# Performance work log

Measured on AMD Instinct MI355X. Metric: run time of the kernel, lower is better.

## Reference

```python
import jax, jax.numpy as jnp
import numpy as np

TEMP = 0.1
GAMMA = 0.75
CHUNK = 300      # hardcoded b=300 in the original forward
EPS = 1e-8
LOSS_WEIGHT = 0.1


def _l2norm(x, axis):
    return x / (jnp.linalg.norm(x, axis=axis, keepdims=True) + 1e-12)


def setup_inputs() -> dict:
    key = jax.random.key(0)
    k = jax.random.split(key, 6)
    B, D, C = 2, 128, 19
    H = W = 240          # full image -> n = 57600 negatives (192 chunks of 300)
    h = w = 60           # overlap crop size -> P = 3600 anchor pixels
    feats_view1 = _l2norm(jax.random.normal(k[0], (B, D, H, W), jnp.float32), axis=1)
    pos_feats1 = _l2norm(jax.random.normal(k[1], (B, D, h, w), jnp.float32), axis=1)
    pos_feats2 = _l2norm(jax.random.normal(k[2], (B, D, h, w), jnp.float32), axis=1)
    pseudo_logits1 = jax.random.uniform(k[3], (B, C, h, w), jnp.float32)
    pseudo_logits2 = jax.random.uniform(k[4], (B, C, h, w), jnp.float32)
    neg_pseudo_logits = jax.random.uniform(k[5], (B, C, H, W), jnp.float32)
    return {
        "feats_view1": feats_view1,
        "pos_feats1": pos_feats1,
        "pos_feats2": pos_feats2,
        "pseudo_logits1": pseudo_logits1,
        "pseudo_logits2": pseudo_logits2,
        "neg_pseudo_logits": neg_pseudo_logits,
    }


def _per_sample(f1, f2, nf, pl1, pl2, npl):
    # f1,f2: [D,h,w] cropped overlap feats; nf: [D,H,W] negatives; pl*: [C,h,w]; npl: [C,H,W]
    D = f1.shape[0]
    C = pl1.shape[0]
    feats1 = f1.reshape(D, -1)                               # [D, P]
    feats2 = jax.lax.stop_gradient(f2.reshape(D, -1))        # detach() in original
    P = feats1.shape[1]
    neg_feats = nf.reshape(D, -1)                            # [D, N]
    N = neg_feats.shape[1]
    labels1 = jnp.argmax(pl1.reshape(C, -1), axis=0)         # [P] anchor pseudo-labels
    neg_labels = jnp.argmax(npl.reshape(C, -1), axis=0)      # [N] negative pseudo-labels

    pos1 = (feats1 * feats2).sum(0) / TEMP                   # [P]

    nchunks = N // CHUNK                                     # N chosen divisible by CHUNK
    nf_c = neg_feats.reshape(D, nchunks, CHUNK).transpose(1, 0, 2)  # [K, D, b]
    nl_c = neg_labels.reshape(nchunks, CHUNK)                       # [K, b]

    def step(acc, xs):
        nfi, nli = xs
        scores = jnp.einsum('dp,db->pb', feats1, nfi) / TEMP        # [P, b]
        mask = (labels1[:, None] != nli[None, :]).astype(scores.dtype)
        return acc + (mask * jnp.exp(scores)).sum(-1), None

    neg_logits, _ = jax.lax.scan(step, jnp.zeros((P,), feats1.dtype), (nf_c, nl_c))

    pos_exp = jnp.exp(pos1)
    lossn = -jnp.log(pos_exp / (pos_exp + neg_logits + EPS) + EPS)  # [P]

    # mask1 = argmax over classes of (dir_mask * pos_mask), as in the original
    combo = ((pl1 < pl2) & (pl2 > GAMMA)).astype(lossn.dtype).reshape(C, -1)
    mask1 = jnp.argmax(combo, axis=0).astype(lossn.dtype)           # [P]
    return (mask1 * lossn).sum() / (mask1.sum() + EPS)


def reference(feats_view1, pos_feats1, pos_feats2, pseudo_logits1, pseudo_logits2, neg_pseudo_logits):
    losses = jax.vmap(_per_sample)(pos_feats1, pos_feats2, feats_view1,
                                   pseudo_logits1, pseudo_logits2, neg_pseudo_logits)
    return LOSS_WEIGHT * (losses[0] + losses[1])
```

## Files before the change

kernel.cpp:

```cpp
#include <hip/hip_runtime.h>
#include <string.h>

#define D_ 128
#define P_ 3600
#define N_ 57600
#define C_ 19
#define NB 2
#define NSPLIT 8
#define TOTCH 450
#define PT 29

typedef short bf16x8 __attribute__((ext_vector_type(8)));
typedef float f32x4 __attribute__((ext_vector_type(4)));

__device__ __forceinline__ ushort f2bf(float x) {
  unsigned u = __float_as_uint(x);
  u = (u + 0x7fffu + ((u >> 16) & 1u)) >> 16;
  return (ushort)u;
}

__device__ __forceinline__ void gload_lds16(const void* g, void* l) {
  __builtin_amdgcn_global_load_lds(
      (const __attribute__((address_space(1))) unsigned int*)g,
      (__attribute__((address_space(3))) unsigned int*)l, 16, 0, 0);
}

__global__ void prep_kernel(const float* __restrict__ XB, ushort* __restrict__ YB,
                            const float* __restrict__ XA, ushort* __restrict__ YA,
                            const float* __restrict__ npl, int* __restrict__ nlab,
                            const float* __restrict__ pl1, const float* __restrict__ pl2,
                            const float* __restrict__ f2,
                            int* __restrict__ lab1, float* __restrict__ mask1,
                            float* __restrict__ pos1, float* __restrict__ neg_logits) {
  __shared__ float T[64][129];
  const int b = blockIdx.y;
  const int tid = threadIdx.x;

  if (blockIdx.x >= N_ / 64 + 57) {
    int p = (blockIdx.x - (N_ / 64 + 57)) * 256 + tid;
    if (p >= P_) return;
    const float* a1 = pl1 + (size_t)b * C_ * P_ + p;
    const float* a2 = pl2 + (size_t)b * C_ * P_ + p;
    float best = a1[0]; int bi = 0;
    int mfirst = ((a1[0] < a2[0]) && (a2[0] > 0.75f)) ? 0 : -1;
#pragma unroll
    for (int c = 1; c < C_; ++c) {
      float v1 = a1[(size_t)c * P_], v2 = a2[(size_t)c * P_];
      if (v1 > best) { best = v1; bi = c; }
      if (mfirst < 0 && (v1 < v2) && (v2 > 0.75f)) mfirst = c;
    }
    lab1[b * P_ + p] = bi;
    mask1[b * P_ + p] = (mfirst < 0) ? 0.0f : (float)mfirst;
    neg_logits[b * P_ + p] = 0.0f;
    const float* g1 = XA + (size_t)b * D_ * P_ + p;
    const float* g2 = f2 + (size_t)b * D_ * P_ + p;
    float s = 0.f;
#pragma unroll 8
    for (int d = 0; d < D_; ++d) s += g1[(size_t)d * P_] * g2[(size_t)d * P_];
    pos1[b * P_ + p] = s * 10.0f;
    return;
  }

  const bool isB = blockIdx.x < (N_ / 64);
  const int M = isB ? N_ : P_;
  const float scale = isB ? 1.0f : 14.4269504089f;
  const int nbase = (isB ? blockIdx.x : (blockIdx.x - N_ / 64)) * 64;
  const float* Xb = (isB ? XB : XA) + (size_t)b * D_ * M;
  ushort* Yb = (isB ? YB : YA) + (size_t)b * M * D_;
  const int nq = tid & 15;
  const int dr = tid >> 4;
#pragma unroll
  for (int i = 0; i < 8; ++i) {
    int d = i * 16 + dr;
    int gn0 = nbase + nq * 4;
    if (gn0 > M - 4) gn0 = M - 4;
    float4 v = *(const float4*)(Xb + (size_t)d * M + gn0);
    T[nq * 4 + 0][d] = v.x;
    T[nq * 4 + 1][d] = v.y;
    T[nq * 4 + 2][d] = v.z;
    T[nq * 4 + 3][d] = v.w;
  }
  __syncthreads();
  const int d0 = (tid & 31) * 4;
#pragma unroll
  for (int i = 0; i < 8; ++i) {
    int n = i * 8 + (tid >> 5);
    int gn = nbase + n;
    if (gn < M) {
      ushort4 u;
      u.x = f2bf(T[n][d0 + 0] * scale);
      u.y = f2bf(T[n][d0 + 1] * scale);
      u.z = f2bf(T[n][d0 + 2] * scale);
      u.w = f2bf(T[n][d0 + 3] * scale);
      *(ushort4*)(Yb + (size_t)gn * D_ + d0) = u;
    }
  }
  if (isB && tid < 64) {
    int gn = nbase + tid;
    const float* base = npl + (size_t)b * C_ * N_ + gn;
    float best = base[0]; int bi = 0;
#pragma unroll
    for (int c = 1; c < C_; ++c) {
      float v = base[(size_t)c * N_];
      if (v > best) { best = v; bi = c; }
    }
    nlab[b * N_ + gn] = bi;
  }
}

__global__ __launch_bounds__(256, 3) void gemm_kernel(
    const ushort* __restrict__ At, const ushort* __restrict__ Bt,
    const int* __restrict__ lab1g, const int* __restrict__ nlabg,
    float* __restrict__ neg_logits) {
  __shared__ __attribute__((aligned(16))) ushort Sh[2][64 * 128];
  const int flat = blockIdx.x;
  const int xcd = flat & 7;
  const int rem = flat >> 3;
  const int slot = rem / PT;
  const int ptile = rem % PT;
  const int g = slot * 8 + xcd;
  const int y = g >> 1;
  const int b = g & 1;

  const int tid = threadIdx.x;
  const int wid = tid >> 6, lane = tid & 63;
  const int quad = lane >> 4, lm = lane & 15;
  const int qr = wid & 1, qc = wid >> 1;
  const ushort* Atb = At + (size_t)b * P_ * D_;
  const ushort* Btb = Bt + (size_t)b * N_ * D_;
  const int* lab1 = lab1g + b * P_;
  const int* nlab = nlabg + b * N_;

  const int row4 = wid * 4 + quad;
  const int cc = lane & 15;
  const int swz = cc ^ (row4 & 7);

#pragma unroll
  for (int i = 0; i < 8; ++i) {
    int row = i * 16 + row4;
    int p = ptile * 128 + row; if (p > P_ - 1) p = P_ - 1;
    gload_lds16(Atb + (size_t)p * D_ + swz * 8, &Sh[0][0] + (i * 16 + wid * 4) * 128);
  }
  __syncthreads();

  bf16x8 af[4][4];
#pragma unroll
  for (int r = 0; r < 4; ++r) {
    int row = qr * 64 + r * 16 + lm;
#pragma unroll
    for (int k0 = 0; k0 < 4; ++k0) {
      int ch = (k0 * 4 + quad) ^ (row & 7);
      af[r][k0] = *(const bf16x8*)(&Sh[0][0] + row * 128 + ch * 8);
    }
  }

  int labp[16];
#pragma unroll
  for (int r = 0; r < 4; ++r)
#pragma unroll
    for (int gg = 0; gg < 4; ++gg) {
      int p = ptile * 128 + qr * 64 + r * 16 + quad * 4 + gg;
      labp[r * 4 + gg] = lab1[p > P_ - 1 ? P_ - 1 : p];
    }

  float rsum[16];
#pragma unroll
  for (int i = 0; i < 16; ++i) rsum[i] = 0.f;
  const f32x4 zero4 = {0.f, 0.f, 0.f, 0.f};

  const int c0 = (y * TOTCH) / NSPLIT;
  const int c1 = ((y + 1) * TOTCH) / NSPLIT;
  const int Hh = (c1 - c0) * 2;
  const ushort* srcB = Btb + (size_t)(c0 * 128 + row4) * D_ + swz * 8;

  __syncthreads();
#pragma unroll
  for (int i = 0; i < 4; ++i)
    gload_lds16(srcB + (size_t)(i * 16) * D_, &Sh[0][(i * 16 + wid * 4) * 128]);

  for (int t = 0; t < Hh; ++t) {
    const int buf = t & 1;
    __syncthreads();
    if (t + 1 < Hh) {
      const ushort* s = srcB + (size_t)((t + 1) * 64) * D_;
#pragma unroll
      for (int i = 0; i < 4; ++i)
        gload_lds16(s + (size_t)(i * 16) * D_, &Sh[buf ^ 1][(i * 16 + wid * 4) * 128]);
    }

    const int nb64 = c0 * 128 + t * 64;
#pragma unroll
    for (int c = 0; c < 2; ++c) {
      const int brow = qc * 32 + c * 16 + lm;
      const int nl = nlab[nb64 + brow];
      f32x4 acc[4];
      {
        int ch = quad ^ (lm & 7);
        bf16x8 bf = *(const bf16x8*)(&Sh[buf][brow * 128 + ch * 8]);
#pragma unroll
        for (int r = 0; r < 4; ++r)
          acc[r] = __builtin_amdgcn_mfma_f32_16x16x32_bf16(af[r][0], bf, zero4, 0, 0, 0);
      }
#pragma unroll
      for (int k0 = 1; k0 < 4; ++k0) {
        int ch = (k0 * 4 + quad) ^ (lm & 7);
        bf16x8 bf = *(const bf16x8*)(&Sh[buf][brow * 128 + ch * 8]);
#pragma unroll
        for (int r = 0; r < 4; ++r)
          acc[r] = __builtin_amdgcn_mfma_f32_16x16x32_bf16(af[r][k0], bf, acc[r], 0, 0, 0);
      }
#pragma unroll
      for (int r = 0; r < 4; ++r)
#pragma unroll
        for (int gg = 0; gg < 4; ++gg) {
          float e = __builtin_amdgcn_exp2f(acc[r][gg]);
          rsum[r * 4 + gg] += (labp[r * 4 + gg] != nl) ? e : 0.f;
        }
    }
  }

#pragma unroll
  for (int i = 0; i < 16; ++i) {
    float v = rsum[i];
    v += __shfl_xor(v, 1);
    v += __shfl_xor(v, 2);
    v += __shfl_xor(v, 4);
    v += __shfl_xor(v, 8);
    rsum[i] = v;
  }
  if (lm == 0) {
#pragma unroll
    for (int r = 0; r < 4; ++r)
#pragma unroll
      for (int gg = 0; gg < 4; ++gg) {
        int p = ptile * 128 + qr * 64 + r * 16 + quad * 4 + gg;
        if (p < P_) atomicAdd(&neg_logits[b * P_ + p], rsum[r * 4 + gg]);
      }
  }
}

__global__ void finalize_kernel(const float* __restrict__ neg_logits,
                                const float* __restrict__ pos1,
                                const float* __restrict__ mask1,
                                float* __restrict__ out) {
  double s1[2] = {0.0, 0.0}, s2[2] = {0.0, 0.0};
  for (int idx = threadIdx.x; idx < NB * P_; idx += 256) {
    int b = idx / P_;
    float ne = neg_logits[idx];
    float pe = __expf(pos1[idx]);
    float l = -logf(pe / (pe + ne + 1e-8f) + 1e-8f);
    float w = mask1[idx];
    s1[b] += (double)(w * l);
    s2[b] += (double)w;
  }
#pragma unroll
  for (int off = 32; off > 0; off >>= 1) {
    s1[0] += __shfl_down(s1[0], off);
    s2[0] += __shfl_down(s2[0], off);
    s1[1] += __shfl_down(s1[1], off);
    s2[1] += __shfl_down(s2[1], off);
  }
  __shared__ double sm[4][4];
  int wid = threadIdx.x >> 6, lane = threadIdx.x & 63;
  if (lane == 0) { sm[wid][0] = s1[0]; sm[wid][1] = s2[0]; sm[wid][2] = s1[1]; sm[wid][3] = s2[1]; }
  __syncthreads();
  if (threadIdx.x == 0) {
    double a = 0, bsum = 0, c = 0, d = 0;
    for (int w = 0; w < 4; ++w) { a += sm[w][0]; bsum += sm[w][1]; c += sm[w][2]; d += sm[w][3]; }
    out[0] = (float)(0.1 * (a / (bsum + 1e-8) + c / (d + 1e-8)));
  }
}

extern "C" void kernel_launch(void* const* d_in, const int* in_sizes, int n_in,
                              void* d_out, int out_size, void* d_ws, size_t ws_size,
                              hipStream_t stream) {
  const float* feats_view1 = (const float*)d_in[0];
  const float* pos_feats1  = (const float*)d_in[1];
  const float* pos_feats2  = (const float*)d_in[2];
  const float* pl1 = (const float*)d_in[3];
  const float* pl2 = (const float*)d_in[4];
  const float* npl = (const float*)d_in[5];

  char* ws = (char*)d_ws;
  ushort* Bt        = (ushort*)(ws + 0);
  ushort* At        = (ushort*)(ws + 29491200);
  int*    nlab      = (int*)   (ws + 31334400);
  int*    lab1      = (int*)   (ws + 31795200);
  float*  mask1     = (float*) (ws + 31824000);
  float*  pos1      = (float*) (ws + 31852800);
  float*  neg_logits= (float*) (ws + 31881600);

  prep_kernel<<<dim3(N_ / 64 + 57 + 15, NB), 256, 0, stream>>>(
      feats_view1, Bt, pos_feats1, At, npl, nlab,
      pl1, pl2, pos_feats2, lab1, mask1, pos1, neg_logits);
  gemm_kernel<<<dim3(8 * 58), 256, 0, stream>>>(At, Bt, lab1, nlab, neg_logits);
  finalize_kernel<<<1, 256, 0, stream>>>(neg_logits, pos1, mask1, (float*)d_out);
}
```

Measured before the change: 276.5 us.

## Load negative features straight from global into registers and split N finer

The double-buffered LDS staging of the negative-feature tiles is removed. Each wave now reads its B fragments directly from global memory into registers before the MFMAs, which drops the per-tile __syncthreads and LDS traffic. The N range is also split 12 ways instead of 8, so the grid grows to 696 blocks. The trade-off is that global-load latency is no longer hidden by explicit prefetching, and pairs of waves fetch the same B rows redundantly through cache.

Result: slower. 531.2 us (+92.1%).

```diff
diff --git a/kernel.cpp b/kernel.cpp
--- a/kernel.cpp
+++ b/kernel.cpp
@@ -6,7 +6,7 @@
 #define N_ 57600
 #define C_ 19
 #define NB 2
-#define NSPLIT 8
+#define NSPLIT 12
 #define TOTCH 450
 #define PT 29
 
@@ -112,12 +112,12 @@
     const ushort* __restrict__ At, const ushort* __restrict__ Bt,
     const int* __restrict__ lab1g, const int* __restrict__ nlabg,
     float* __restrict__ neg_logits) {
-  __shared__ __attribute__((aligned(16))) ushort Sh[2][64 * 128];
+  __shared__ __attribute__((aligned(16))) ushort Sh[128 * 128];
   const int flat = blockIdx.x;
   const int xcd = flat & 7;
-  const int rem = flat >> 3;
-  const int slot = rem / PT;
-  const int ptile = rem % PT;
+  const int idx = flat >> 3;
+  const int slot = idx / PT;
+  const int ptile = idx % PT;
   const int g = slot * 8 + xcd;
   const int y = g >> 1;
   const int b = g & 1;
@@ -139,7 +139,7 @@
   for (int i = 0; i < 8; ++i) {
     int row = i * 16 + row4;
     int p = ptile * 128 + row; if (p > P_ - 1) p = P_ - 1;
-    gload_lds16(Atb + (size_t)p * D_ + swz * 8, &Sh[0][0] + (i * 16 + wid * 4) * 128);
+    gload_lds16(Atb + (size_t)p * D_ + swz * 8, &Sh[(i * 16 + wid * 4) * 128]);
   }
   __syncthreads();
 
@@ -150,7 +150,7 @@
 #pragma unroll
     for (int k0 = 0; k0 < 4; ++k0) {
       int ch = (k0 * 4 + quad) ^ (row & 7);
-      af[r][k0] = *(const bf16x8*)(&Sh[0][0] + row * 128 + ch * 8);
+      af[r][k0] = *(const bf16x8*)(&Sh[row * 128 + ch * 8]);
     }
   }
 
@@ -170,45 +170,30 @@
 
   const int c0 = (y * TOTCH) / NSPLIT;
   const int c1 = ((y + 1) * TOTCH) / NSPLIT;
-  const int Hh = (c1 - c0) * 2;
-  const ushort* srcB = Btb + (size_t)(c0 * 128 + row4) * D_ + swz * 8;
-
-  __syncthreads();
-#pragma unroll
-  for (int i = 0; i < 4; ++i)
-    gload_lds16(srcB + (size_t)(i * 16) * D_, &Sh[0][(i * 16 + wid * 4) * 128]);
-
-  for (int t = 0; t < Hh; ++t) {
-    const int buf = t & 1;
-    __syncthreads();
-    if (t + 1 < Hh) {
-      const ushort* s = srcB + (size_t)((t + 1) * 64) * D_;
-#pragma unroll
-      for (int i = 0; i < 4; ++i)
-        gload_lds16(s + (size_t)(i * 16) * D_, &Sh[buf ^ 1][(i * 16 + wid * 4) * 128]);
-    }
-
-    const int nb64 = c0 * 128 + t * 64;
-#pragma unroll
-    for (int c = 0; c < 2; ++c) {
-      const int brow = qc * 32 + c * 16 + lm;
-      const int nl = nlab[nb64 + brow];
+
+  for (int j = c0; j < c1; ++j) {
+#pragma unroll
+    for (int c = 0; c < 4; ++c) {
+      const int brow = j * 128 + qc * 64 + c * 16 + lm;
+      const ushort* Bp = Btb + (size_t)brow * D_ + quad * 8;
+      bf16x8 bf0 = *(const bf16x8*)(Bp);
+      bf16x8 bf1 = *(const bf16x8*)(Bp + 32);
+      bf16x8 bf2 = *(const bf16x8*)(Bp + 64);
+      bf16x8 bf3 = *(const bf16x8*)(Bp + 96);
+      const int nl = nlab[brow];
       f32x4 acc[4];
-      {
-        int ch = quad ^ (lm & 7);
-        bf16x8 bf = *(const bf16x8*)(&Sh[buf][brow * 128 + ch * 8]);
-#pragma unroll
-        for (int r = 0; r < 4; ++r)
-          acc[r] = __builtin_amdgcn_mfma_f32_16x16x32_bf16(af[r][0], bf, zero4, 0, 0, 0);
-      }
-#pragma unroll
-      for (int k0 = 1; k0 < 4; ++k0) {
-        int ch = (k0 * 4 + quad) ^ (lm & 7);
-        bf16x8 bf = *(const bf16x8*)(&Sh[buf][brow * 128 + ch * 8]);
-#pragma unroll
-        for (int r = 0; r < 4; ++r)
-          acc[r] = __builtin_amdgcn_mfma_f32_16x16x32_bf16(af[r][k0], bf, acc[r], 0, 0, 0);
-      }
+#pragma unroll
+      for (int r = 0; r < 4; ++r)
+        acc[r] = __builtin_amdgcn_mfma_f32_16x16x32_bf16(af[r][0], bf0, zero4, 0, 0, 0);
+#pragma unroll
+      for (int r = 0; r < 4; ++r)
+        acc[r] = __builtin_amdgcn_mfma_f32_16x16x32_bf16(af[r][1], bf1, acc[r], 0, 0, 0);
+#pragma unroll
+      for (int r = 0; r < 4; ++r)
+        acc[r] = __builtin_amdgcn_mfma_f32_16x16x32_bf16(af[r][2], bf2, acc[r], 0, 0, 0);
+#pragma unroll
+      for (int r = 0; r < 4; ++r)
+        acc[r] = __builtin_amdgcn_mfma_f32_16x16x32_bf16(af[r][3], bf3, acc[r], 0, 0, 0);
 #pragma unroll
       for (int r = 0; r < 4; ++r)
 #pragma unroll
@@ -293,6 +278,6 @@
   prep_kernel<<<dim3(N_ / 64 + 57 + 15, NB), 256, 0, stream>>>(
       feats_view1, Bt, pos_feats1, At, npl, nlab,
       pl1, pl2, pos_feats2, lab1, mask1, pos1, neg_logits);
-  gemm_kernel<<<dim3(8 * 58), 256, 0, stream>>>(At, Bt, lab1, nlab, neg_logits);
+  gemm_kernel<<<dim3(8 * 3 * PT), 256, 0, stream>>>(At, Bt, lab1, nlab, neg_logits);
   finalize_kernel<<<1, 256, 0, stream>>>(neg_logits, pos1, mask1, (float*)d_out);
 }
```
